# Kernel tuning notes

Hardware: AMD Instinct MI355X
Metric: run time of the kernel (lower is better)

Reference implementation:

```python
import jax, jax.numpy as jnp
import numpy as np

N = 16384      # nodes
E = 262144     # edges (avg degree 16)
F_IN = 128     # n_feat
D = 128        # n_dims
C = 10         # n_clss
SIGMA = 1.0    # args.sigma


def setup_inputs() -> dict:
    key = jax.random.key(0)
    ks = jax.random.split(key, 12)
    s_in = 1.0 / np.sqrt(F_IN)
    s_d = 1.0 / np.sqrt(D)
    s_c = 1.0 / np.sqrt(2 * D)
    return {
        "x": jax.random.normal(ks[0], (N, F_IN), jnp.float32),
        "edge_index": jax.random.randint(ks[1], (2, E), 0, N, dtype=jnp.int32),
        # SAGEConv1: lin_l (neighbors, with bias) and lin_r (root, no bias)
        "W1l": jax.random.normal(ks[2], (D, F_IN), jnp.float32) * s_in,
        "b1l": jnp.zeros((D,), jnp.float32),
        "W1r": jax.random.normal(ks[3], (D, F_IN), jnp.float32) * s_in,
        # SAGEConv2
        "W2l": jax.random.normal(ks[4], (D, D), jnp.float32) * s_d,
        "b2l": jnp.zeros((D,), jnp.float32),
        "W2r": jax.random.normal(ks[5], (D, D), jnp.float32) * s_d,
        # anchor vector (init.uniform_ -> U[0,1))
        "aux": jax.random.uniform(ks[6], (D,), jnp.float32),
        # classifier on [h, z] concat
        "Wc": jax.random.normal(ks[7], (C, 2 * D), jnp.float32) * s_c,
        "bc": jnp.zeros((C,), jnp.float32),
    }


def _sage_conv(x, src, dst, Wl, bl, Wr):
    # PyG SAGEConv (mean aggr): out = lin_l(mean_{j in N(i)} x_j) + lin_r(x_i)
    msg = x[src]                                                  # [E, d]
    agg = jax.ops.segment_sum(msg, dst, num_segments=N)           # [N, d]
    deg = jax.ops.segment_sum(jnp.ones((src.shape[0],), x.dtype), dst,
                              num_segments=N)                     # [N]
    agg = agg / jnp.maximum(deg, 1.0)[:, None]
    return agg @ Wl.T + bl + x @ Wr.T


def _kernel_aggregate(h, aux, sigma):
    # cosine similarity to anchor (torch eps = 1e-8)
    eps = 1e-8
    hn = jnp.maximum(jnp.linalg.norm(h, axis=-1), eps)            # [N]
    an = jnp.maximum(jnp.linalg.norm(aux), eps)
    score = (h @ aux) / (hn * an)                                 # [N]
    diff = score[None, :] - score[:, None]                        # [N, N]
    kappa = jnp.exp(-(diff * diff) / (sigma * sigma))             # [N, N]
    return (kappa @ h) / jnp.sum(kappa, axis=1, keepdims=True)    # [N, d]


def reference(x, W1l, b1l, W1r, W2l, b2l, W2r, aux, Wc, bc, edge_index):
    src, dst = edge_index[0], edge_index[1]
    h = jax.nn.relu(_sage_conv(x, src, dst, W1l, b1l, W1r))
    # dropout is identity at inference
    h = _sage_conv(h, src, dst, W2l, b2l, W2r)
    z = _kernel_aggregate(h, aux, SIGMA)
    return jnp.concatenate([h, z], axis=-1) @ Wc.T + bc           # [N, C]
```

## Files before the change

### kernel.cpp

```cpp
#include <hip/hip_runtime.h>
#include <hip/hip_bf16.h>

#define D 128
#define KTERMS 16
#define ECAP 768

typedef __attribute__((ext_vector_type(8))) short bf16x8;
typedef __attribute__((ext_vector_type(4))) float f32x4;

__device__ inline short rne_bf16(float f) {
    union { float f; unsigned u; } v; v.f = f;
    unsigned r = (v.u + 0x7fffu + ((v.u >> 16) & 1u)) >> 16;
    return (short)r;
}
__device__ inline float bf16_to_f(unsigned s) {
    union { unsigned u; float f; } v; v.u = s << 16;
    return v.f;
}
__device__ inline unsigned pk2(float a, float b) {
    return (unsigned)(unsigned short)rne_bf16(a) | ((unsigned)(unsigned short)rne_bf16(b) << 16);
}
__device__ inline void addv(float* acc, uint4 v) {
    acc[0] += bf16_to_f(v.x & 0xffffu);
    acc[1] += bf16_to_f(v.x >> 16);
    acc[2] += bf16_to_f(v.y & 0xffffu);
    acc[3] += bf16_to_f(v.y >> 16);
    acc[4] += bf16_to_f(v.z & 0xffffu);
    acc[5] += bf16_to_f(v.z >> 16);
    acc[6] += bf16_to_f(v.w & 0xffffu);
    acc[7] += bf16_to_f(v.w >> 16);
}

__global__ __launch_bounds__(256) void prep_kernel(const float* __restrict__ x,
                                                   short* __restrict__ xb,
                                                   const float* __restrict__ W1l,
                                                   const float* __restrict__ W1r,
                                                   const float* __restrict__ W2l,
                                                   const float* __restrict__ W2r,
                                                   short* __restrict__ Bc1,
                                                   short* __restrict__ Bc2,
                                                   int* __restrict__ zero_ints,
                                                   float* __restrict__ zero_f) {
    int b = blockIdx.x;
    int tid = threadIdx.x;
    if (b < 1024) {
        int base = (b * 256 + tid) * 8;
        const float4 a = *reinterpret_cast<const float4*>(&x[base]);
        const float4 c = *reinterpret_cast<const float4*>(&x[base + 4]);
        uint4 o;
        o.x = pk2(a.x, a.y);
        o.y = pk2(a.z, a.w);
        o.z = pk2(c.x, c.y);
        o.w = pk2(c.z, c.w);
        *reinterpret_cast<uint4*>(&xb[base]) = o;
    } else if (b < 1280) {
        int idx = (b - 1024) * 256 + tid;
        int layer = idx >> 15;
        int rem = idx & 32767;
        int c = rem >> 8, k = rem & 255;
        const float* Wl = layer ? W2l : W1l;
        const float* Wr = layer ? W2r : W1r;
        float v = (k < 128) ? Wl[c * 128 + k] : Wr[c * 128 + (k - 128)];
        short* Bc = layer ? Bc2 : Bc1;
        Bc[c * 256 + k] = rne_bf16(v);
    } else if (b < 1312) {
        int idx = (b - 1280) * 256 + tid;
        reinterpret_cast<int4*>(zero_ints)[idx] = make_int4(0, 0, 0, 0);
    } else {
        for (int e = tid; e < KTERMS * D + KTERMS; e += 256) zero_f[e] = 0.0f;
    }
}

__global__ __launch_bounds__(256) void degi_kernel(const int* __restrict__ dst,
                                                   int* __restrict__ degi, int E) {
    int e = blockIdx.x * 256 + threadIdx.x;
    if (e < E) atomicAdd(&degi[dst[e]], 1);
}

__global__ __launch_bounds__(1024) void scan_kernel(const int* __restrict__ degi,
                                                    int* __restrict__ rowptr,
                                                    float* __restrict__ invdeg, int N) {
    __shared__ int part[1024];
    int tid = threadIdx.x;
    int base = tid * 16;
    int loc[16];
    int s = 0;
#pragma unroll
    for (int i = 0; i < 16; i++) {
        int d = degi[base + i];
        loc[i] = s; s += d;
        invdeg[base + i] = 1.0f / fmaxf((float)d, 1.0f);
    }
    part[tid] = s;
    __syncthreads();
    for (int off = 1; off < 1024; off <<= 1) {
        int t = (tid >= off) ? part[tid - off] : 0;
        __syncthreads();
        if (tid >= off) part[tid] += t;
        __syncthreads();
    }
    int prefix = part[tid] - s;
#pragma unroll
    for (int i = 0; i < 16; i++) rowptr[base + i] = prefix + loc[i];
    if (tid == 1023) rowptr[N] = prefix + s;
}

__global__ __launch_bounds__(256) void fill_kernel(const int* __restrict__ src,
                                                   const int* __restrict__ dst,
                                                   const int* __restrict__ rowptr,
                                                   int* __restrict__ cursor,
                                                   int* __restrict__ csr_src, int E) {
    int e = blockIdx.x * 256 + threadIdx.x;
    if (e < E) {
        int d = dst[e];
        int pos = atomicAdd(&cursor[d], 1);
        csr_src[rowptr[d] + pos] = src[e];
    }
}

template <int RELU, int SCORE>
__global__ __launch_bounds__(256) void sage_fused_kernel(const short* __restrict__ Asrc,
                                                         const short* __restrict__ Bc,
                                                         const float* __restrict__ bias,
                                                         const int* __restrict__ rowptr,
                                                         const int* __restrict__ csr_src,
                                                         const float* __restrict__ invdeg,
                                                         const float* __restrict__ aux,
                                                         short* __restrict__ outb,
                                                         float* __restrict__ outf,
                                                         float* __restrict__ sbuf,
                                                         float* __restrict__ wbuf) {
    __shared__ short aggl[16 * 128];
    __shared__ int eidx[ECAP];
    __shared__ float sdot[16][4];
    __shared__ float snrm[16][4];
    __shared__ float an_s;

    int tid = threadIdx.x;
    int lane = tid & 63;
    int wid = tid >> 6;
    int row0 = blockIdx.x * 16;
    int sub = lane >> 4, sl = lane & 15;

    int eb = rowptr[row0];
    int ecnt = rowptr[row0 + 16] - eb;
    for (int e = tid; e < ecnt && e < ECAP; e += 256) eidx[e] = csr_src[eb + e];

    if (SCORE && wid == 0) {
        float2 av = *reinterpret_cast<const float2*>(&aux[lane * 2]);
        float na = av.x * av.x + av.y * av.y;
        for (int m = 1; m < 64; m <<= 1) na += __shfl_xor(na, m);
        if (lane == 0) an_s = fmaxf(sqrtf(na), 1e-8f);
    }
    __syncthreads();

    int r = wid * 4 + sub;
    int node = row0 + r;
    int beg = rowptr[node], end = rowptr[node + 1];
    float inv = invdeg[node];
    float acc8[8] = {0.0f, 0.0f, 0.0f, 0.0f, 0.0f, 0.0f, 0.0f, 0.0f};
    int j = beg;
    for (; j + 3 < end; j += 4) {
        int jj = j - eb;
        int s0, s1, s2, s3;
        if (jj + 3 < ECAP) {
            s0 = eidx[jj]; s1 = eidx[jj + 1]; s2 = eidx[jj + 2]; s3 = eidx[jj + 3];
        } else {
            s0 = csr_src[j]; s1 = csr_src[j + 1]; s2 = csr_src[j + 2]; s3 = csr_src[j + 3];
        }
        uint4 v0 = *reinterpret_cast<const uint4*>(&Asrc[(size_t)s0 * D + sl * 8]);
        uint4 v1 = *reinterpret_cast<const uint4*>(&Asrc[(size_t)s1 * D + sl * 8]);
        uint4 v2 = *reinterpret_cast<const uint4*>(&Asrc[(size_t)s2 * D + sl * 8]);
        uint4 v3 = *reinterpret_cast<const uint4*>(&Asrc[(size_t)s3 * D + sl * 8]);
        addv(acc8, v0); addv(acc8, v1); addv(acc8, v2); addv(acc8, v3);
    }
    for (; j < end; j++) {
        int jj = j - eb;
        int s = (jj < ECAP) ? eidx[jj] : csr_src[j];
        uint4 v = *reinterpret_cast<const uint4*>(&Asrc[(size_t)s * D + sl * 8]);
        addv(acc8, v);
    }
    uint4 o;
    o.x = pk2(acc8[0] * inv, acc8[1] * inv);
    o.y = pk2(acc8[2] * inv, acc8[3] * inv);
    o.z = pk2(acc8[4] * inv, acc8[5] * inv);
    o.w = pk2(acc8[6] * inv, acc8[7] * inv);
    int wbyte = (r * 256 + sl * 16) ^ ((r & 7) << 4);
    *reinterpret_cast<uint4*>(reinterpret_cast<char*>(aggl) + wbyte) = o;
    __syncthreads();

    int colbase = wid * 32;
    int rl = lane & 15;
    int kg = lane >> 4;
    int koff = kg * 8;
    int arow_g = row0 + rl;

    f32x4 acc[2];
    acc[0] = (f32x4){0.0f, 0.0f, 0.0f, 0.0f};
    acc[1] = (f32x4){0.0f, 0.0f, 0.0f, 0.0f};

#pragma unroll
    for (int kc = 0; kc < 8; kc++) {
        bf16x8 a;
        if (kc < 4) {
            int rbyte = (rl * 256 + kc * 64 + kg * 16) ^ ((rl & 7) << 4);
            a = *reinterpret_cast<const bf16x8*>(reinterpret_cast<const char*>(aggl) + rbyte);
        } else {
            int k = (kc - 4) * 32 + koff;
            a = *reinterpret_cast<const bf16x8*>(&Asrc[(size_t)arow_g * D + k]);
        }
#pragma unroll
        for (int t = 0; t < 2; t++) {
            int col = colbase + t * 16 + rl;
            bf16x8 b = *reinterpret_cast<const bf16x8*>(&Bc[(size_t)col * 256 + kc * 32 + koff]);
            acc[t] = __builtin_amdgcn_mfma_f32_16x16x32_bf16(a, b, acc[t], 0, 0, 0);
        }
    }

    int rbase = kg * 4;
    float dotp[4] = {0.0f, 0.0f, 0.0f, 0.0f};
    float nrmp[4] = {0.0f, 0.0f, 0.0f, 0.0f};
#pragma unroll
    for (int t = 0; t < 2; t++) {
        int col = colbase + t * 16 + rl;
        float bv = bias[col];
        float av = SCORE ? aux[col] : 0.0f;
#pragma unroll
        for (int rr = 0; rr < 4; rr++) {
            float v = acc[t][rr] + bv;
            if (RELU) v = fmaxf(v, 0.0f);
            int grow = row0 + rbase + rr;
            if (outf) outf[(size_t)grow * D + col] = v;
            else outb[(size_t)grow * D + col] = rne_bf16(v);
            dotp[rr] += v * av;
            nrmp[rr] += v * v;
        }
    }

    if (SCORE) {
#pragma unroll
        for (int m = 1; m < 16; m <<= 1) {
#pragma unroll
            for (int rr = 0; rr < 4; rr++) {
                dotp[rr] += __shfl_xor(dotp[rr], m);
                nrmp[rr] += __shfl_xor(nrmp[rr], m);
            }
        }
        if (rl == 0) {
#pragma unroll
            for (int rr = 0; rr < 4; rr++) {
                sdot[rbase + rr][wid] = dotp[rr];
                snrm[rbase + rr][wid] = nrmp[rr];
            }
        }
        __syncthreads();
        if (tid < 16) {
            float dot = sdot[tid][0] + sdot[tid][1] + sdot[tid][2] + sdot[tid][3];
            float nh  = snrm[tid][0] + snrm[tid][1] + snrm[tid][2] + snrm[tid][3];
            float hn = fmaxf(sqrtf(nh), 1e-8f);
            float sc = dot / (hn * an_s);
            sbuf[row0 + tid] = sc;
            wbuf[row0 + tid] = expf(-sc * sc);
        }
    }
}

__global__ __launch_bounds__(512) void moments_kernel(const float* __restrict__ h,
                                                      const float* __restrict__ sbuf,
                                                      const float* __restrict__ wbuf,
                                                      float* __restrict__ M,
                                                      float* __restrict__ mden, int N) {
    __shared__ float lds[8 * KTERMS * D];
    __shared__ float ldsm[8 * KTERMS];
    int tid = threadIdx.x;
    int w = tid >> 6, lane = tid & 63;
    int j0 = blockIdx.x * 64 + w * 8;

    float2 acc[KTERMS];
    float macc[KTERMS];
#pragma unroll
    for (int k = 0; k < KTERMS; k++) { acc[k] = make_float2(0.0f, 0.0f); macc[k] = 0.0f; }

    for (int j = j0; j < j0 + 8; j++) {
        float sj = sbuf[j];
        float wj = wbuf[j];
        float2 hv = *reinterpret_cast<const float2*>(&h[(size_t)j * D + lane * 2]);
        float coef = wj;
#pragma unroll
        for (int k = 0; k < KTERMS; k++) {
            acc[k].x += coef * hv.x;
            acc[k].y += coef * hv.y;
            macc[k] += coef;
            coef *= sj;
        }
    }

#pragma unroll
    for (int k = 0; k < KTERMS; k++) {
        lds[(w * KTERMS + k) * D + lane * 2]     = acc[k].x;
        lds[(w * KTERMS + k) * D + lane * 2 + 1] = acc[k].y;
    }
    if (lane == 0) {
#pragma unroll
        for (int k = 0; k < KTERMS; k++) ldsm[w * KTERMS + k] = macc[k];
    }
    __syncthreads();

    for (int e = tid; e < KTERMS * D; e += 512) {
        float s = 0.0f;
#pragma unroll
        for (int ww = 0; ww < 8; ww++) s += lds[ww * KTERMS * D + e];
        atomicAdd(&M[e], s);
    }
    if (tid < KTERMS) {
        float s = 0.0f;
#pragma unroll
        for (int ww = 0; ww < 8; ww++) s += ldsm[ww * KTERMS + tid];
        atomicAdd(&mden[tid], s);
    }
}

__global__ __launch_bounds__(128) void zcls_kernel(const float* __restrict__ M,
                                                   const float* __restrict__ mden,
                                                   const float* __restrict__ sbuf,
                                                   const float* __restrict__ h,
                                                   const float* __restrict__ Wc,
                                                   const float* __restrict__ bc,
                                                   float* __restrict__ out, int N) {
    const float A[KTERMS] = {1.0f, 2.0f, 2.0f, 1.3333334f, 0.6666667f, 0.26666668f,
                             0.08888889f, 0.025396826f, 0.0063492064f, 0.0014109347f,
                             2.8218695e-4f, 5.1306718e-5f, 8.5511196e-6f, 1.3155569e-6f,
                             1.8793670e-7f, 2.5058226e-8f};
    __shared__ float Ml[KTERMS * D];
    __shared__ float ml[KTERMS];
    __shared__ float wls[10 * 256];
    __shared__ float red[10][2];
    int tid = threadIdx.x;
    int lane = tid & 63, w = tid >> 6;
#pragma unroll
    for (int k = 0; k < KTERMS; k++) Ml[k * D + tid] = M[k * D + tid];
    if (tid < KTERMS) ml[tid] = mden[tid];
    for (int e = tid; e < 10 * 256; e += 128) wls[e] = Wc[e];
    __syncthreads();

    int n0 = blockIdx.x * 16;
    for (int n = n0; n < n0 + 16; n++) {
        float si = sbuf[n];
        float num = 0.0f, den = 0.0f, p = 1.0f;
#pragma unroll
        for (int k = 0; k < KTERMS; k++) {
            float ck = A[k] * p;
            num += ck * Ml[k * D + tid];
            den += ck * ml[k];
            p *= si;
        }
        float zc = num / den;
        float hc = h[(size_t)n * D + tid];

        float part[10];
#pragma unroll
        for (int c = 0; c < 10; c++)
            part[c] = hc * wls[c * 256 + tid] + zc * wls[c * 256 + 128 + tid];
#pragma unroll
        for (int m = 1; m < 64; m <<= 1) {
#pragma unroll
            for (int c = 0; c < 10; c++) part[c] += __shfl_xor(part[c], m);
        }
        if (lane == 0) {
#pragma unroll
            for (int c = 0; c < 10; c++) red[c][w] = part[c];
        }
        __syncthreads();
        if (tid < 10) out[(size_t)n * 10 + tid] = red[tid][0] + red[tid][1] + bc[tid];
        __syncthreads();
    }
}

extern "C" void kernel_launch(void* const* d_in, const int* in_sizes, int n_in,
                              void* d_out, int out_size, void* d_ws, size_t ws_size,
                              hipStream_t stream) {
    const float* x   = (const float*)d_in[0];
    const int*   ei  = (const int*)d_in[1];
    const float* W1l = (const float*)d_in[2];
    const float* b1l = (const float*)d_in[3];
    const float* W1r = (const float*)d_in[4];
    const float* W2l = (const float*)d_in[5];
    const float* b2l = (const float*)d_in[6];
    const float* W2r = (const float*)d_in[7];
    const float* aux = (const float*)d_in[8];
    const float* Wc  = (const float*)d_in[9];
    const float* bc  = (const float*)d_in[10];
    float* out = (float*)d_out;

    const int N = in_sizes[0] / D;
    const int E = in_sizes[1] / 2;
    const int* srcArr = ei;
    const int* dstArr = ei + E;
    const size_t ND = (size_t)N * D;

    int* ip = (int*)d_ws;
    int* degi    = ip; ip += N;
    int* cursor  = ip; ip += N;
    int* rowptr  = ip; ip += N + 1;
    int* csr_src = ip; ip += E;
    uintptr_t up = ((uintptr_t)ip + 15) & ~(uintptr_t)15;
    short* sp = (short*)up;
    short* xb   = sp; sp += ND;
    short* h1b  = sp; sp += ND;
    short* Bc1  = sp; sp += 128 * 256;
    short* Bc2  = sp; sp += 128 * 256;
    up = ((uintptr_t)sp + 15) & ~(uintptr_t)15;
    float* p = (float*)up;
    float* invdeg = p; p += N;
    float* sbuf   = p; p += N;
    float* wbuf   = p; p += N;
    float* M      = p; p += KTERMS * D;
    float* mden   = p; p += KTERMS;
    float* h2     = p; p += ND;

    prep_kernel<<<1313, 256, 0, stream>>>(x, xb, W1l, W1r, W2l, W2r, Bc1, Bc2, degi, M);

    degi_kernel<<<(E + 255) / 256, 256, 0, stream>>>(dstArr, degi, E);
    scan_kernel<<<1, 1024, 0, stream>>>(degi, rowptr, invdeg, N);
    fill_kernel<<<(E + 255) / 256, 256, 0, stream>>>(srcArr, dstArr, rowptr, cursor, csr_src, E);

    sage_fused_kernel<1, 0><<<N / 16, 256, 0, stream>>>(xb, Bc1, b1l, rowptr, csr_src, invdeg,
                                                        aux, h1b, nullptr, nullptr, nullptr);
    sage_fused_kernel<0, 1><<<N / 16, 256, 0, stream>>>(h1b, Bc2, b2l, rowptr, csr_src, invdeg,
                                                        aux, nullptr, h2, sbuf, wbuf);

    moments_kernel<<<N / 64, 512, 0, stream>>>(h2, sbuf, wbuf, M, mden, N);

    zcls_kernel<<<N / 16, 128, 0, stream>>>(M, mden, sbuf, h2, Wc, bc, out, N);
}
```

Measured before the change: 132.9 us.

## Double SAGE block to 512 threads, halving per-thread gather width and MFMA columns

The fused SAGE kernel now runs 512 threads per 16-row block. Each node's neighbor gather uses 32 lanes loading 8 bytes each instead of 16 lanes loading 16 bytes, and each of the 8 waves computes 16 output columns with one MFMA chain instead of 32 columns with two. The aim is more memory-level parallelism and occupancy in the latency-bound gather. In exchange, the loads are narrower, the block is larger, and each A fragment is reloaded by twice as many waves.

```diff
diff --git a/kernel.cpp b/kernel.cpp
--- a/kernel.cpp
+++ b/kernel.cpp
@@ -20,15 +20,11 @@
 __device__ inline unsigned pk2(float a, float b) {
     return (unsigned)(unsigned short)rne_bf16(a) | ((unsigned)(unsigned short)rne_bf16(b) << 16);
 }
-__device__ inline void addv(float* acc, uint4 v) {
+__device__ inline void addv2(float* acc, uint2 v) {
     acc[0] += bf16_to_f(v.x & 0xffffu);
     acc[1] += bf16_to_f(v.x >> 16);
     acc[2] += bf16_to_f(v.y & 0xffffu);
     acc[3] += bf16_to_f(v.y >> 16);
-    acc[4] += bf16_to_f(v.z & 0xffffu);
-    acc[5] += bf16_to_f(v.z >> 16);
-    acc[6] += bf16_to_f(v.w & 0xffffu);
-    acc[7] += bf16_to_f(v.w >> 16);
 }
 
 __global__ __launch_bounds__(256) void prep_kernel(const float* __restrict__ x,
@@ -119,7 +115,7 @@
 }
 
 template <int RELU, int SCORE>
-__global__ __launch_bounds__(256) void sage_fused_kernel(const short* __restrict__ Asrc,
+__global__ __launch_bounds__(512) void sage_fused_kernel(const short* __restrict__ Asrc,
                                                          const short* __restrict__ Bc,
                                                          const float* __restrict__ bias,
                                                          const int* __restrict__ rowptr,
@@ -132,19 +128,18 @@
                                                          float* __restrict__ wbuf) {
     __shared__ short aggl[16 * 128];
     __shared__ int eidx[ECAP];
-    __shared__ float sdot[16][4];
-    __shared__ float snrm[16][4];
+    __shared__ float sdot[16][8];
+    __shared__ float snrm[16][8];
     __shared__ float an_s;
 
     int tid = threadIdx.x;
     int lane = tid & 63;
     int wid = tid >> 6;
     int row0 = blockIdx.x * 16;
-    int sub = lane >> 4, sl = lane & 15;
 
     int eb = rowptr[row0];
     int ecnt = rowptr[row0 + 16] - eb;
-    for (int e = tid; e < ecnt && e < ECAP; e += 256) eidx[e] = csr_src[eb + e];
+    for (int e = tid; e < ecnt && e < ECAP; e += 512) eidx[e] = csr_src[eb + e];
 
     if (SCORE && wid == 0) {
         float2 av = *reinterpret_cast<const float2*>(&aux[lane * 2]);
@@ -154,11 +149,12 @@
     }
     __syncthreads();
 
-    int r = wid * 4 + sub;
+    int r = tid >> 5;
+    int g32 = tid & 31;
     int node = row0 + r;
     int beg = rowptr[node], end = rowptr[node + 1];
     float inv = invdeg[node];
-    float acc8[8] = {0.0f, 0.0f, 0.0f, 0.0f, 0.0f, 0.0f, 0.0f, 0.0f};
+    float acc4[4] = {0.0f, 0.0f, 0.0f, 0.0f};
     int j = beg;
     for (; j + 3 < end; j += 4) {
         int jj = j - eb;
@@ -168,36 +164,34 @@
         } else {
             s0 = csr_src[j]; s1 = csr_src[j + 1]; s2 = csr_src[j + 2]; s3 = csr_src[j + 3];
         }
-        uint4 v0 = *reinterpret_cast<const uint4*>(&Asrc[(size_t)s0 * D + sl * 8]);
-        uint4 v1 = *reinterpret_cast<const uint4*>(&Asrc[(size_t)s1 * D + sl * 8]);
-        uint4 v2 = *reinterpret_cast<const uint4*>(&Asrc[(size_t)s2 * D + sl * 8]);
-        uint4 v3 = *reinterpret_cast<const uint4*>(&Asrc[(size_t)s3 * D + sl * 8]);
-        addv(acc8, v0); addv(acc8, v1); addv(acc8, v2); addv(acc8, v3);
+        uint2 v0 = *reinterpret_cast<const uint2*>(&Asrc[(size_t)s0 * D + g32 * 4]);
+        uint2 v1 = *reinterpret_cast<const uint2*>(&Asrc[(size_t)s1 * D + g32 * 4]);
+        uint2 v2 = *reinterpret_cast<const uint2*>(&Asrc[(size_t)s2 * D + g32 * 4]);
+        uint2 v3 = *reinterpret_cast<const uint2*>(&Asrc[(size_t)s3 * D + g32 * 4]);
+        addv2(acc4, v0); addv2(acc4, v1); addv2(acc4, v2); addv2(acc4, v3);
     }
     for (; j < end; j++) {
         int jj = j - eb;
         int s = (jj < ECAP) ? eidx[jj] : csr_src[j];
-        uint4 v = *reinterpret_cast<const uint4*>(&Asrc[(size_t)s * D + sl * 8]);
-        addv(acc8, v);
-    }
-    uint4 o;
-    o.x = pk2(acc8[0] * inv, acc8[1] * inv);
-    o.y = pk2(acc8[2] * inv, acc8[3] * inv);
-    o.z = pk2(acc8[4] * inv, acc8[5] * inv);
-    o.w = pk2(acc8[6] * inv, acc8[7] * inv);
-    int wbyte = (r * 256 + sl * 16) ^ ((r & 7) << 4);
-    *reinterpret_cast<uint4*>(reinterpret_cast<char*>(aggl) + wbyte) = o;
+        uint2 v = *reinterpret_cast<const uint2*>(&Asrc[(size_t)s * D + g32 * 4]);
+        addv2(acc4, v);
+    }
+    {
+        uint2 o;
+        o.x = pk2(acc4[0] * inv, acc4[1] * inv);
+        o.y = pk2(acc4[2] * inv, acc4[3] * inv);
+        int wbyte = (r * 256 + g32 * 8) ^ ((r & 7) << 4);
+        *reinterpret_cast<uint2*>(reinterpret_cast<char*>(aggl) + wbyte) = o;
+    }
     __syncthreads();
 
-    int colbase = wid * 32;
+    int colbase = wid * 16;
     int rl = lane & 15;
     int kg = lane >> 4;
     int koff = kg * 8;
     int arow_g = row0 + rl;
 
-    f32x4 acc[2];
-    acc[0] = (f32x4){0.0f, 0.0f, 0.0f, 0.0f};
-    acc[1] = (f32x4){0.0f, 0.0f, 0.0f, 0.0f};
+    f32x4 acc = (f32x4){0.0f, 0.0f, 0.0f, 0.0f};
 
 #pragma unroll
     for (int kc = 0; kc < 8; kc++) {
@@ -209,32 +203,25 @@
             int k = (kc - 4) * 32 + koff;
             a = *reinterpret_cast<const bf16x8*>(&Asrc[(size_t)arow_g * D + k]);
         }
-#pragma unroll
-        for (int t = 0; t < 2; t++) {
-            int col = colbase + t * 16 + rl;
-            bf16x8 b = *reinterpret_cast<const bf16x8*>(&Bc[(size_t)col * 256 + kc * 32 + koff]);
-            acc[t] = __builtin_amdgcn_mfma_f32_16x16x32_bf16(a, b, acc[t], 0, 0, 0);
-        }
+        int col = colbase + rl;
+        bf16x8 b = *reinterpret_cast<const bf16x8*>(&Bc[(size_t)col * 256 + kc * 32 + koff]);
+        acc = __builtin_amdgcn_mfma_f32_16x16x32_bf16(a, b, acc, 0, 0, 0);
     }
 
     int rbase = kg * 4;
-    float dotp[4] = {0.0f, 0.0f, 0.0f, 0.0f};
-    float nrmp[4] = {0.0f, 0.0f, 0.0f, 0.0f};
-#pragma unroll
-    for (int t = 0; t < 2; t++) {
-        int col = colbase + t * 16 + rl;
-        float bv = bias[col];
-        float av = SCORE ? aux[col] : 0.0f;
-#pragma unroll
-        for (int rr = 0; rr < 4; rr++) {
-            float v = acc[t][rr] + bv;
-            if (RELU) v = fmaxf(v, 0.0f);
-            int grow = row0 + rbase + rr;
-            if (outf) outf[(size_t)grow * D + col] = v;
-            else outb[(size_t)grow * D + col] = rne_bf16(v);
-            dotp[rr] += v * av;
-            nrmp[rr] += v * v;
-        }
+    int col = colbase + rl;
+    float bv = bias[col];
+    float av = SCORE ? aux[col] : 0.0f;
+    float dotp[4], nrmp[4];
+#pragma unroll
+    for (int rr = 0; rr < 4; rr++) {
+        float v = acc[rr] + bv;
+        if (RELU) v = fmaxf(v, 0.0f);
+        int grow = row0 + rbase + rr;
+        if (outf) outf[(size_t)grow * D + col] = v;
+        else outb[(size_t)grow * D + col] = rne_bf16(v);
+        dotp[rr] = v * av;
+        nrmp[rr] = v * v;
     }
 
     if (SCORE) {
@@ -255,8 +242,9 @@
         }
         __syncthreads();
         if (tid < 16) {
-            float dot = sdot[tid][0] + sdot[tid][1] + sdot[tid][2] + sdot[tid][3];
-            float nh  = snrm[tid][0] + snrm[tid][1] + snrm[tid][2] + snrm[tid][3];
+            float dot = 0.0f, nh = 0.0f;
+#pragma unroll
+            for (int ww = 0; ww < 8; ww++) { dot += sdot[tid][ww]; nh += snrm[tid][ww]; }
             float hn = fmaxf(sqrtf(nh), 1e-8f);
             float sc = dot / (hn * an_s);
             sbuf[row0 + tid] = sc;
@@ -424,9 +412,9 @@
     scan_kernel<<<1, 1024, 0, stream>>>(degi, rowptr, invdeg, N);
     fill_kernel<<<(E + 255) / 256, 256, 0, stream>>>(srcArr, dstArr, rowptr, cursor, csr_src, E);
 
-    sage_fused_kernel<1, 0><<<N / 16, 256, 0, stream>>>(xb, Bc1, b1l, rowptr, csr_src, invdeg,
+    sage_fused_kernel<1, 0><<<N / 16, 512, 0, stream>>>(xb, Bc1, b1l, rowptr, csr_src, invdeg,
                                                         aux, h1b, nullptr, nullptr, nullptr);
-    sage_fused_kernel<0, 1><<<N / 16, 256, 0, stream>>>(h1b, Bc2, b2l, rowptr, csr_src, invdeg,
+    sage_fused_kernel<0, 1><<<N / 16, 512, 0, stream>>>(h1b, Bc2, b2l, rowptr, csr_src, invdeg,
                                                         aux, nullptr, h2, sbuf, wbuf);
 
     moments_kernel<<<N / 64, 512, 0, stream>>>(h2, sbuf, wbuf, M, mden, N);
```

New measurement: 138.6 us. 1.04x slower.

## Balance neighbor aggregation by splitting block edges evenly across thread groups

Applied to the files above, without the earlier changes.

The neighbor gather no longer maps one 16-lane group to one node. The block's edge range is split into 16 equal chunks, one per group, and each group accumulates partial row sums that are merged into a float shared-memory buffer with atomic adds. This aims to remove the load imbalance caused by uneven node degrees within a block. It costs a zero-initialised 8KB float buffer, LDS atomics at every row boundary, and an extra sync plus conversion pass.

```diff
diff --git a/kernel.cpp b/kernel.cpp
--- a/kernel.cpp
+++ b/kernel.cpp
@@ -131,7 +131,9 @@
                                                          float* __restrict__ sbuf,
                                                          float* __restrict__ wbuf) {
     __shared__ short aggl[16 * 128];
+    __shared__ float aggf[16 * 128];
     __shared__ int eidx[ECAP];
+    __shared__ int rptr_l[17];
     __shared__ float sdot[16][4];
     __shared__ float snrm[16][4];
     __shared__ float an_s;
@@ -140,11 +142,14 @@
     int lane = tid & 63;
     int wid = tid >> 6;
     int row0 = blockIdx.x * 16;
-    int sub = lane >> 4, sl = lane & 15;
+    int q = tid >> 4;
+    int sl = tid & 15;
 
     int eb = rowptr[row0];
     int ecnt = rowptr[row0 + 16] - eb;
     for (int e = tid; e < ecnt && e < ECAP; e += 256) eidx[e] = csr_src[eb + e];
+    if (tid < 17) rptr_l[tid] = rowptr[row0 + tid] - eb;
+    for (int e = tid; e < 16 * 128; e += 256) aggf[e] = 0.0f;
 
     if (SCORE && wid == 0) {
         float2 av = *reinterpret_cast<const float2*>(&aux[lane * 2]);
@@ -154,39 +159,56 @@
     }
     __syncthreads();
 
-    int r = wid * 4 + sub;
-    int node = row0 + r;
-    int beg = rowptr[node], end = rowptr[node + 1];
-    float inv = invdeg[node];
-    float acc8[8] = {0.0f, 0.0f, 0.0f, 0.0f, 0.0f, 0.0f, 0.0f, 0.0f};
-    int j = beg;
-    for (; j + 3 < end; j += 4) {
-        int jj = j - eb;
-        int s0, s1, s2, s3;
-        if (jj + 3 < ECAP) {
-            s0 = eidx[jj]; s1 = eidx[jj + 1]; s2 = eidx[jj + 2]; s3 = eidx[jj + 3];
-        } else {
-            s0 = csr_src[j]; s1 = csr_src[j + 1]; s2 = csr_src[j + 2]; s3 = csr_src[j + 3];
-        }
-        uint4 v0 = *reinterpret_cast<const uint4*>(&Asrc[(size_t)s0 * D + sl * 8]);
-        uint4 v1 = *reinterpret_cast<const uint4*>(&Asrc[(size_t)s1 * D + sl * 8]);
-        uint4 v2 = *reinterpret_cast<const uint4*>(&Asrc[(size_t)s2 * D + sl * 8]);
-        uint4 v3 = *reinterpret_cast<const uint4*>(&Asrc[(size_t)s3 * D + sl * 8]);
-        addv(acc8, v0); addv(acc8, v1); addv(acc8, v2); addv(acc8, v3);
-    }
-    for (; j < end; j++) {
-        int jj = j - eb;
-        int s = (jj < ECAP) ? eidx[jj] : csr_src[j];
-        uint4 v = *reinterpret_cast<const uint4*>(&Asrc[(size_t)s * D + sl * 8]);
-        addv(acc8, v);
-    }
-    uint4 o;
-    o.x = pk2(acc8[0] * inv, acc8[1] * inv);
-    o.y = pk2(acc8[2] * inv, acc8[3] * inv);
-    o.z = pk2(acc8[4] * inv, acc8[5] * inv);
-    o.w = pk2(acc8[6] * inv, acc8[7] * inv);
-    int wbyte = (r * 256 + sl * 16) ^ ((r & 7) << 4);
-    *reinterpret_cast<uint4*>(reinterpret_cast<char*>(aggl) + wbyte) = o;
+    {
+        int s = (ecnt + 15) >> 4;
+        int eq0 = q * s; if (eq0 > ecnt) eq0 = ecnt;
+        int eq1 = eq0 + s; if (eq1 > ecnt) eq1 = ecnt;
+        if (eq0 < eq1) {
+            int r = 0;
+            while (r < 15 && rptr_l[r + 1] <= eq0) r++;
+            int j = eq0;
+            float acc8[8] = {0.0f, 0.0f, 0.0f, 0.0f, 0.0f, 0.0f, 0.0f, 0.0f};
+            while (j < eq1) {
+                int rend = rptr_l[r + 1]; if (rend > eq1) rend = eq1;
+                for (; j + 3 < rend; j += 4) {
+                    int s0 = (j     < ECAP) ? eidx[j]     : csr_src[eb + j];
+                    int s1 = (j + 1 < ECAP) ? eidx[j + 1] : csr_src[eb + j + 1];
+                    int s2 = (j + 2 < ECAP) ? eidx[j + 2] : csr_src[eb + j + 2];
+                    int s3 = (j + 3 < ECAP) ? eidx[j + 3] : csr_src[eb + j + 3];
+                    uint4 v0 = *reinterpret_cast<const uint4*>(&Asrc[(size_t)s0 * D + sl * 8]);
+                    uint4 v1 = *reinterpret_cast<const uint4*>(&Asrc[(size_t)s1 * D + sl * 8]);
+                    uint4 v2 = *reinterpret_cast<const uint4*>(&Asrc[(size_t)s2 * D + sl * 8]);
+                    uint4 v3 = *reinterpret_cast<const uint4*>(&Asrc[(size_t)s3 * D + sl * 8]);
+                    addv(acc8, v0); addv(acc8, v1); addv(acc8, v2); addv(acc8, v3);
+                }
+                for (; j < rend; j++) {
+                    int ss = (j < ECAP) ? eidx[j] : csr_src[eb + j];
+                    uint4 v = *reinterpret_cast<const uint4*>(&Asrc[(size_t)ss * D + sl * 8]);
+                    addv(acc8, v);
+                }
+#pragma unroll
+                for (int u = 0; u < 8; u++) {
+                    atomicAdd(&aggf[r * 128 + sl * 8 + u], acc8[u]);
+                    acc8[u] = 0.0f;
+                }
+                r++;
+            }
+        }
+    }
+    __syncthreads();
+
+    {
+        int row = tid >> 4;
+        float inv = invdeg[row0 + row];
+        const float* af = &aggf[row * 128 + sl * 8];
+        uint4 o;
+        o.x = pk2(af[0] * inv, af[1] * inv);
+        o.y = pk2(af[2] * inv, af[3] * inv);
+        o.z = pk2(af[4] * inv, af[5] * inv);
+        o.w = pk2(af[6] * inv, af[7] * inv);
+        int wbyte = (row * 256 + sl * 16) ^ ((row & 7) << 4);
+        *reinterpret_cast<uint4*>(reinterpret_cast<char*>(aggl) + wbyte) = o;
+    }
     __syncthreads();
 
     int colbase = wid * 32;
```

After: 168.4 us. 1.27x slower.
